# Performance work log

Measured on AMD Instinct MI355X. Metric: run time of the kernel, lower is better.

Reference implementation:

```python
import jax, jax.numpy as jnp
import numpy as np

EMBED = 768
HEADS = 12
DEPTH = 12
FEAT = 2048


def _ln(x, w, b, eps=1e-6):
    m = x.mean(-1, keepdims=True)
    v = ((x - m) ** 2).mean(-1, keepdims=True)
    return (x - m) * jax.lax.rsqrt(v + eps) * w + b


def _var_attn(x, mbias, Wqkv, bqkv, Wp, bp, h, f):
    # x: (B, N, D) with N = 1 + f*n ; mbias: (B, N) additive mask (0 or -100)
    B, N, D = x.shape
    d = D // h
    n = (N - 1) // f
    scale = d ** -0.5
    qkv = x @ Wqkv.T + bqkv
    q, k, v = jnp.split(qkv, 3, axis=-1)
    hd = lambda t: t.reshape(B, N, h, d).transpose(0, 2, 1, 3)  # (B,h,N,d)
    q = hd(q) * scale
    k = hd(k)
    v = hd(v)
    # cls token attends to everything
    cls_sim = jnp.einsum('bhd,bhjd->bhj', q[:, :, 0], k) + mbias[:, None, :]
    cls_out = jnp.einsum('bhj,bhjd->bhd', jax.nn.softmax(cls_sim, axis=-1), v)[:, :, None, :]
    # spatial tokens attend within their frame plus the cls token
    q_ = q[:, :, 1:].reshape(B, h, f, n, d)
    k_ = jnp.concatenate([jnp.broadcast_to(k[:, :, None, 0:1, :], (B, h, f, 1, d)),
                          k[:, :, 1:].reshape(B, h, f, n, d)], axis=3)
    v_ = jnp.concatenate([jnp.broadcast_to(v[:, :, None, 0:1, :], (B, h, f, 1, d)),
                          v[:, :, 1:].reshape(B, h, f, n, d)], axis=3)
    mcat = jnp.concatenate([jnp.broadcast_to(mbias[:, 0][:, None, None], (B, f, 1)),
                            mbias[:, 1:].reshape(B, f, n)], axis=2)  # (B,f,n+1)
    sim = jnp.einsum('bhfid,bhfjd->bhfij', q_, k_) + mcat[:, None, :, None, :]
    out = jnp.einsum('bhfij,bhfjd->bhfid', jax.nn.softmax(sim, axis=-1), v_)
    out = out.reshape(B, h, f * n, d)
    out = jnp.concatenate([cls_out, out], axis=2).transpose(0, 2, 1, 3).reshape(B, N, D)
    return out @ Wp.T + bp


def setup_inputs() -> dict:
    key = jax.random.key(0)
    ks = jax.random.split(key, 12)
    B, F, L = 256, 4, 20
    std = 0.02
    p = {}
    p['x'] = jax.random.normal(ks[0], (B, F, L, 2054), dtype=jnp.float32)
    p['x_mask'] = jax.random.randint(ks[1], (B, F, L), 0, 2, dtype=jnp.int32)
    p['obj_W'] = (jax.random.normal(ks[2], (EMBED, FEAT)) * std).astype(jnp.float32)
    p['obj_b'] = jnp.zeros((EMBED,), jnp.float32)
    p['pos_W'] = (jax.random.normal(ks[3], (EMBED, 6)) * std).astype(jnp.float32)
    p['pos_b'] = jnp.zeros((EMBED,), jnp.float32)
    p['cls_token'] = (jax.random.normal(ks[4], (1, 1, EMBED)) * std).astype(jnp.float32)
    p['cls_pos'] = (jax.random.normal(ks[5], (1, L + 1, EMBED)) * std).astype(jnp.float32)
    p['temporal_embed'] = jnp.zeros((1, F, EMBED), jnp.float32)
    p['ln1_w'] = jnp.ones((DEPTH, EMBED), jnp.float32)
    p['ln1_b'] = jnp.zeros((DEPTH, EMBED), jnp.float32)
    p['ln2_w'] = jnp.ones((DEPTH, EMBED), jnp.float32)
    p['ln2_b'] = jnp.zeros((DEPTH, EMBED), jnp.float32)
    p['qkv_W'] = (jax.random.normal(ks[6], (DEPTH, 3 * EMBED, EMBED)) * std).astype(jnp.float32)
    p['qkv_b'] = jnp.zeros((DEPTH, 3 * EMBED), jnp.float32)
    p['ap_W'] = (jax.random.normal(ks[7], (DEPTH, EMBED, EMBED)) * std).astype(jnp.float32)
    p['ap_b'] = jnp.zeros((DEPTH, EMBED), jnp.float32)
    p['fc1_W'] = (jax.random.normal(ks[8], (DEPTH, 4 * EMBED, EMBED)) * std).astype(jnp.float32)
    p['fc1_b'] = jnp.zeros((DEPTH, 4 * EMBED), jnp.float32)
    p['fc2_W'] = (jax.random.normal(ks[9], (DEPTH, EMBED, 4 * EMBED)) * std).astype(jnp.float32)
    p['fc2_b'] = jnp.zeros((DEPTH, EMBED), jnp.float32)
    p['proj_W'] = (jax.random.normal(ks[10], (256, EMBED)) * std).astype(jnp.float32)
    return p


def reference(x, x_mask, obj_W, obj_b, pos_W, pos_b, cls_token, cls_pos, temporal_embed,
              ln1_w, ln1_b, ln2_w, ln2_b, qkv_W, qkv_b, ap_W, ap_b,
              fc1_W, fc1_b, fc2_W, fc2_b, proj_W):
    B, F, L, _ = x.shape
    tok = x[..., :FEAT] @ obj_W.T + obj_b + (x[..., FEAT:] @ pos_W.T + pos_b)
    tok = tok.reshape(B, F * L, EMBED)
    m = x_mask.reshape(B, F * L).astype(tok.dtype)
    tok = jnp.concatenate([jnp.broadcast_to(cls_token, (B, 1, EMBED)), tok], axis=1)
    m = jnp.concatenate([jnp.ones((B, 1), tok.dtype), m], axis=1)
    mbias = (m - 1.0) * 100.0  # 0 for valid, -100 for padded
    pos_total = jnp.concatenate([cls_pos[:, 0:1, :], jnp.repeat(temporal_embed, L, axis=1)], axis=1)
    tok = tok + pos_total

    def body(xc, p):
        l1w, l1b, qW, qb, aW, ab, l2w, l2b, f1W, f1b, f2W, f2b = p
        a = _var_attn(_ln(xc, l1w, l1b), mbias, qW, qb, aW, ab, HEADS, F)
        xr = xc + a
        xc = xr + (jax.nn.gelu(_ln(xr, l2w, l2b) @ f1W.T + f1b, approximate=False) @ f2W.T + f2b)
        return xc, None

    tok, _ = jax.lax.scan(body, tok, (ln1_w, ln1_b, qkv_W, qkv_b, ap_W, ap_b,
                                      ln2_w, ln2_b, fc1_W, fc1_b, fc2_W, fc2_b))
    return tok @ proj_W.T, mbias
```

## Files before the change

### kernel.cpp

```cpp
#include <hip/hip_runtime.h>

typedef __bf16 bf16;
typedef __bf16 bf16x8 __attribute__((ext_vector_type(8)));
typedef float f32x4 __attribute__((ext_vector_type(4)));

#define EMBED 768
#define HEADS 12
#define DEPTH 12
#define B_ 256
#define F_ 4
#define L_ 20
#define NTOK 81
#define ROWS (B_ * NTOK)
#define SROWS (B_ * F_ * L_)

#define GLOAD16(g, l)                                                              \
    __builtin_amdgcn_global_load_lds((const __attribute__((address_space(1))) void*)(g), \
                                     (__attribute__((address_space(3))) void*)(l), 16, 0, 0)

__device__ __forceinline__ float fast_gelu(float v) {
    float x = v * 0.70710678118654752f;
    float ax = fabsf(x);
    float t = __fdividef(1.f, fmaf(0.3275911f, ax, 1.f));
    float p = ((((1.061405429f * t - 1.453152027f) * t + 1.421413741f) * t -
                0.284496736f) * t + 0.254829592f) * t;
    float e = __expf(-ax * ax);
    float erfv = copysignf(1.f - p * e, x);
    return 0.5f * v * (1.f + erfv);
}

__global__ __launch_bounds__(256) void repack_kernel(const float* __restrict__ x,
                                                     bf16* __restrict__ xr) {
    int row = blockIdx.x;
    const float* src = x + (size_t)row * 2054;
    bf16* dst = xr + (size_t)row * 2048;
    int t = threadIdx.x;
    int e0 = t * 8;
    bf16 tmp[8];
#pragma unroll
    for (int i = 0; i < 4; ++i) {
        float2 v = *(const float2*)&src[e0 + 2 * i];
        tmp[2 * i] = (bf16)v.x;
        tmp[2 * i + 1] = (bf16)v.y;
    }
    *(uint4*)&dst[e0] = *(const uint4*)tmp;
}

__global__ __launch_bounds__(256) void w2bf_kernel(const float* __restrict__ src,
                                                   bf16* __restrict__ dst) {
    size_t i = ((size_t)blockIdx.x * 256 + threadIdx.x) * 8;
    float4 a = *(const float4*)&src[i];
    float4 b = *(const float4*)&src[i + 4];
    bf16 t[8] = {(bf16)a.x, (bf16)a.y, (bf16)a.z, (bf16)a.w,
                 (bf16)b.x, (bf16)b.y, (bf16)b.z, (bf16)b.w};
    *(uint4*)&dst[i] = *(const uint4*)t;
}

template <int FUSE, bool ROWMAP, typename CT>
__global__ __launch_bounds__(256) void gemm_bb(const bf16* __restrict__ A, int lda,
                                               const bf16* __restrict__ W,
                                               const float* __restrict__ bias,
                                               const bf16* __restrict__ R,
                                               CT* __restrict__ C, int N, int K) {
    __shared__ __align__(16) char smem[32768];

    const int tid = threadIdx.x;
    const int lane = tid & 63;
    const int wv = tid >> 6;
    const int wm = (wv & 1) * 64;
    const int wn = (wv >> 1) * 64;
    const int lr = lane & 15;
    const int lq = lane >> 4;

    const int GX = gridDim.x;
    const int nwg = GX * gridDim.y;
    const int flat = blockIdx.y * GX + blockIdx.x;
    const int xcd = flat & 7, pos = flat >> 3;
    const int qc = nwg >> 3, rc = nwg & 7;
    const int wg = (xcd < rc ? xcd * (qc + 1) : rc * (qc + 1) + (xcd - rc) * qc) + pos;
    const int n0 = (wg % GX) * 128;
    const int m0 = (wg / GX) * 128;

    const int srow = lane >> 3;
    const int scol = 8 * ((lane & 7) ^ srow);
    const bf16* aB = A + (size_t)(m0 + srow) * lda + scol;
    const bf16* wB = W + (size_t)(n0 + srow) * K + scol;

    bf16* As = (bf16*)smem;
    bf16* Ws = (bf16*)(smem + 16384);

    f32x4 acc[4][4];
#pragma unroll
    for (int i = 0; i < 4; ++i)
#pragma unroll
        for (int j = 0; j < 4; ++j) acc[i][j] = (f32x4){0.f, 0.f, 0.f, 0.f};

    const int swz = (lr & 7) << 4;

    for (int k0 = 0; k0 < K; k0 += 64) {
#pragma unroll
        for (int i = 0; i < 4; ++i) {
            const int ch = wv * 4 + i;
            GLOAD16(aB + (size_t)(ch * 8) * lda + k0, smem + ch * 1024);
            GLOAD16(wB + (size_t)(ch * 8) * K + k0, smem + 16384 + ch * 1024);
        }
        __syncthreads();
#pragma unroll
        for (int kk = 0; kk < 2; ++kk) {
            const int co = (((kk << 6) | (lq << 4)) ^ swz) >> 1;
            bf16x8 af[4], bw[4];
#pragma unroll
            for (int t = 0; t < 4; ++t) {
                af[t] = *(const bf16x8*)&As[(wm + t * 16 + lr) * 64 + co];
                bw[t] = *(const bf16x8*)&Ws[(wn + t * 16 + lr) * 64 + co];
            }
#pragma unroll
            for (int mi = 0; mi < 4; ++mi)
#pragma unroll
                for (int ni = 0; ni < 4; ++ni)
                    acc[mi][ni] = __builtin_amdgcn_mfma_f32_16x16x32_bf16(af[mi], bw[ni],
                                                                          acc[mi][ni], 0, 0, 0);
        }
        __syncthreads();
    }

    float* patch = (float*)(smem + wv * 4352);
    float bv4[4];
#pragma unroll
    for (int ni = 0; ni < 4; ++ni) bv4[ni] = bias ? bias[n0 + wn + ni * 16 + lr] : 0.f;
    const int rr = lane >> 3;
    const int c8 = (lane & 7) * 8;
#pragma unroll
    for (int mi = 0; mi < 4; ++mi) {
#pragma unroll
        for (int ni = 0; ni < 4; ++ni)
#pragma unroll
            for (int r = 0; r < 4; ++r)
                patch[(lq * 4 + r) * 68 + ni * 16 + lr] = acc[mi][ni][r] + bv4[ni];
#pragma unroll
        for (int hf = 0; hf < 2; ++hf) {
            int row = rr + hf * 8;
            float v[8];
            *(float4*)&v[0] = *(const float4*)&patch[row * 68 + c8];
            *(float4*)&v[4] = *(const float4*)&patch[row * 68 + c8 + 4];
            int grow = m0 + wm + mi * 16 + row;
            int gcol = n0 + wn + c8;
            if (FUSE == 1) {
#pragma unroll
                for (int q = 0; q < 8; ++q) v[q] = fast_gelu(v[q]);
            }
            if (FUSE == 2) {
                bf16x8 rv = *(const bf16x8*)&R[(size_t)grow * N + gcol];
#pragma unroll
                for (int q = 0; q < 8; ++q) v[q] += (float)rv[q];
            }
            int orow = grow;
            if (ROWMAP) orow = grow + grow / 80 + 1;
            if constexpr (sizeof(CT) == 2) {
                bf16 ob[8];
#pragma unroll
                for (int q = 0; q < 8; ++q) ob[q] = (bf16)v[q];
                *(uint4*)&C[(size_t)orow * N + gcol] = *(const uint4*)ob;
            } else {
                *(float4*)&C[(size_t)orow * N + gcol] = *(const float4*)&v[0];
                *(float4*)&C[(size_t)orow * N + gcol + 4] = *(const float4*)&v[4];
            }
        }
    }
}

template <int FUSE, bool ROWMAP, typename CT>
__global__ __launch_bounds__(256) void gemm_bt(const bf16* __restrict__ A, int lda,
                                               const float* __restrict__ W,
                                               const float* __restrict__ bias,
                                               const bf16* __restrict__ R,
                                               CT* __restrict__ C, int N, int K) {
    __shared__ __align__(16) bf16 As[128][32];
    __shared__ __align__(16) bf16 Ws[128][32];

    const int tid = threadIdx.x;
    const int lane = tid & 63;
    const int wv = tid >> 6;
    const int wm = (wv & 1) * 64;
    const int wn = (wv >> 1) * 64;
    const int lr = lane & 15;
    const int lq = lane >> 4;
    const int m0 = blockIdx.x * 128;
    const int n0 = blockIdx.y * 128;

    f32x4 acc[4][4];
#pragma unroll
    for (int i = 0; i < 4; ++i)
#pragma unroll
        for (int j = 0; j < 4; ++j) acc[i][j] = (f32x4){0.f, 0.f, 0.f, 0.f};

    for (int k0 = 0; k0 < K; k0 += 32) {
#pragma unroll
        for (int i = 0; i < 2; ++i) {
            int c = tid + 256 * i;
            int row = c >> 2;
            int kc = (c & 3) * 8;
            *(uint4*)&As[row][kc] = *(const uint4*)&A[(size_t)(m0 + row) * lda + k0 + kc];
        }
#pragma unroll
        for (int i = 0; i < 4; ++i) {
            int c = tid + 256 * i;
            int row = c >> 3;
            int kc = (c & 7) * 4;
            float4 v = *(const float4*)&W[(size_t)(n0 + row) * K + k0 + kc];
            bf16 wb[4] = {(bf16)v.x, (bf16)v.y, (bf16)v.z, (bf16)v.w};
            *(uint2*)&Ws[row][kc] = *(const uint2*)wb;
        }
        __syncthreads();
        bf16x8 af[4], bf_[4];
#pragma unroll
        for (int t = 0; t < 4; ++t) {
            af[t] = *(const bf16x8*)&As[wm + t * 16 + lr][lq * 8];
            bf_[t] = *(const bf16x8*)&Ws[wn + t * 16 + lr][lq * 8];
        }
#pragma unroll
        for (int mi = 0; mi < 4; ++mi)
#pragma unroll
            for (int ni = 0; ni < 4; ++ni)
                acc[mi][ni] = __builtin_amdgcn_mfma_f32_16x16x32_bf16(af[mi], bf_[ni],
                                                                      acc[mi][ni], 0, 0, 0);
        __syncthreads();
    }

#pragma unroll
    for (int mi = 0; mi < 4; ++mi) {
#pragma unroll
        for (int ni = 0; ni < 4; ++ni) {
            int gcol = n0 + wn + ni * 16 + lr;
            float bv = bias ? bias[gcol] : 0.f;
#pragma unroll
            for (int r = 0; r < 4; ++r) {
                int grow = m0 + wm + mi * 16 + lq * 4 + r;
                float v = acc[mi][ni][r] + bv;
                if (FUSE == 1) v = fast_gelu(v);
                if (FUSE == 2) v += (float)R[(size_t)grow * N + gcol];
                int orow = grow;
                if (ROWMAP) orow = grow + grow / 80 + 1;
                C[(size_t)orow * N + gcol] = (CT)v;
            }
        }
    }
}

__global__ __launch_bounds__(256) void embed_finish(const float* __restrict__ x,
                                                    const float* __restrict__ posW,
                                                    const float* __restrict__ posb,
                                                    const float* __restrict__ temb,
                                                    bf16* __restrict__ tok) {
    int r = blockIdx.x;
    int fr = (r % 80) / 20;
    int orow = r + r / 80 + 1;
    __shared__ float pf[6];
    if (threadIdx.x < 6) pf[threadIdx.x] = x[(size_t)r * 2054 + 2048 + threadIdx.x];
    __syncthreads();
    int t = threadIdx.x;
#pragma unroll
    for (int i = 0; i < 3; ++i) {
        int c = t + 256 * i;
        float v = posb[c] + temb[fr * EMBED + c];
#pragma unroll
        for (int j = 0; j < 6; ++j) v += pf[j] * posW[c * 6 + j];
        size_t idx = (size_t)orow * EMBED + c;
        tok[idx] = (bf16)((float)tok[idx] + v);
    }
}

__global__ __launch_bounds__(256) void cls_mbias_kernel(const float* __restrict__ cls_tok,
                                                        const float* __restrict__ cls_pos,
                                                        const int* __restrict__ xmask,
                                                        bf16* __restrict__ tok,
                                                        float* __restrict__ mbias,
                                                        float* __restrict__ out1) {
    int b = blockIdx.x;
    int t = threadIdx.x;
#pragma unroll
    for (int i = 0; i < 3; ++i) {
        int c = t + 256 * i;
        tok[(size_t)(b * NTOK) * EMBED + c] = (bf16)(cls_tok[c] + cls_pos[c]);
    }
    if (t < NTOK) {
        float mv = (t == 0) ? 0.f : ((float)xmask[b * 80 + t - 1] - 1.f) * 100.f;
        mbias[b * NTOK + t] = mv;
        out1[b * NTOK + t] = mv;
    }
}

__global__ __launch_bounds__(256) void ln_kernel(const bf16* __restrict__ X,
                                                 const float* __restrict__ w,
                                                 const float* __restrict__ b,
                                                 bf16* __restrict__ Y) {
    int half = threadIdx.x >> 7;
    int row = blockIdx.x * 2 + half;
    int tt = threadIdx.x & 127;
    float xv[8];
    float s = 0.f, ss = 0.f;
    if (tt < 96) {
        bf16x8 v8 = *(const bf16x8*)&X[(size_t)row * EMBED + tt * 8];
#pragma unroll
        for (int i = 0; i < 8; ++i) {
            float v = (float)v8[i];
            xv[i] = v;
            s += v;
            ss += v * v;
        }
    }
#pragma unroll
    for (int off = 32; off; off >>= 1) {
        s += __shfl_down(s, off);
        ss += __shfl_down(ss, off);
    }
    __shared__ float ws_s[4], ws_q[4];
    int wv = threadIdx.x >> 6, lane = threadIdx.x & 63;
    if (lane == 0) { ws_s[wv] = s; ws_q[wv] = ss; }
    __syncthreads();
    s = ws_s[half * 2] + ws_s[half * 2 + 1];
    ss = ws_q[half * 2] + ws_q[half * 2 + 1];
    float mean = s * (1.f / 768.f);
    float var = ss * (1.f / 768.f) - mean * mean;
    float inv = rsqrtf(fmaxf(var, 0.f) + 1e-6f);
    if (tt < 96) {
        float4 w0 = *(const float4*)&w[tt * 8];
        float4 w1 = *(const float4*)&w[tt * 8 + 4];
        float4 b0 = *(const float4*)&b[tt * 8];
        float4 b1 = *(const float4*)&b[tt * 8 + 4];
        float wr[8] = {w0.x, w0.y, w0.z, w0.w, w1.x, w1.y, w1.z, w1.w};
        float br[8] = {b0.x, b0.y, b0.z, b0.w, b1.x, b1.y, b1.z, b1.w};
        bf16 ob[8];
#pragma unroll
        for (int i = 0; i < 8; ++i) ob[i] = (bf16)((xv[i] - mean) * inv * wr[i] + br[i]);
        *(uint4*)&Y[(size_t)row * EMBED + tt * 8] = *(const uint4*)ob;
    }
}

__global__ __launch_bounds__(256) void attn_kernel(const bf16* __restrict__ qkv,
                                                   const float* __restrict__ mbias,
                                                   bf16* __restrict__ aout) {
    int bh = blockIdx.x;
    int b = bh / HEADS, h = bh % HEADS;
    __shared__ __align__(16) float Qf[NTOK][68];
    __shared__ __align__(16) float Kf[NTOK][68];
    __shared__ __align__(16) bf16 Vs[NTOK][72];
    __shared__ float S[80][22];
    __shared__ float Sc[96];
    __shared__ float MB[NTOK];
    const size_t base = (size_t)(b * NTOK) * 2304 + h * 64;
    int t = threadIdx.x;

    for (int ch = t; ch < NTOK * 8; ch += 256) {
        int r = ch >> 3, c8 = (ch & 7) * 8;
        size_t o = base + (size_t)r * 2304 + c8;
        bf16x8 qv = *(const bf16x8*)&qkv[o];
        bf16x8 kv = *(const bf16x8*)&qkv[o + 768];
        *(uint4*)&Vs[r][c8] = *(const uint4*)&qkv[o + 1536];
        float4 q0 = {(float)qv[0], (float)qv[1], (float)qv[2], (float)qv[3]};
        float4 q1 = {(float)qv[4], (float)qv[5], (float)qv[6], (float)qv[7]};
        float4 k0 = {(float)kv[0], (float)kv[1], (float)kv[2], (float)kv[3]};
        float4 k1 = {(float)kv[4], (float)kv[5], (float)kv[6], (float)kv[7]};
        *(float4*)&Qf[r][c8] = q0;
        *(float4*)&Qf[r][c8 + 4] = q1;
        *(float4*)&Kf[r][c8] = k0;
        *(float4*)&Kf[r][c8 + 4] = k1;
    }
    if (t < NTOK) MB[t] = mbias[b * NTOK + t];
    __syncthreads();

    {
        int qt;
        if (t < 240) {
            qt = 1 + t / 3;
        } else {
            qt = 0;
        }
        float fq[64];
#pragma unroll
        for (int i = 0; i < 16; ++i) {
            float4 v = *(const float4*)&Qf[qt][i * 4];
            fq[4 * i] = v.x; fq[4 * i + 1] = v.y; fq[4 * i + 2] = v.z; fq[4 * i + 3] = v.w;
        }
        if (t < 240) {
            int qi = t / 3, fb = (qi / 20) * 20, kst = t - qi * 3;
            for (int kj = kst; kj < 21; kj += 3) {
                int kt = (kj == 0) ? 0 : fb + kj;
                float acc = 0.f;
#pragma unroll
                for (int i = 0; i < 16; ++i) {
                    float4 kv = *(const float4*)&Kf[kt][i * 4];
                    acc += fq[4 * i] * kv.x + fq[4 * i + 1] * kv.y +
                           fq[4 * i + 2] * kv.z + fq[4 * i + 3] * kv.w;
                }
                S[qi][kj] = acc * 0.125f + MB[kt];
            }
        } else {
            for (int kt = t - 240; kt < NTOK; kt += 16) {
                float acc = 0.f;
#pragma unroll
                for (int i = 0; i < 16; ++i) {
                    float4 kv = *(const float4*)&Kf[kt][i * 4];
                    acc += fq[4 * i] * kv.x + fq[4 * i + 1] * kv.y +
                           fq[4 * i + 2] * kv.z + fq[4 * i + 3] * kv.w;
                }
                Sc[kt] = acc * 0.125f + MB[kt];
            }
        }
    }
    __syncthreads();

    if (t < 80) {
        float mx = -1e30f;
        for (int j = 0; j < 21; ++j) mx = fmaxf(mx, S[t][j]);
        float sum = 0.f;
        for (int j = 0; j < 21; ++j) { float e = __expf(S[t][j] - mx); S[t][j] = e; sum += e; }
        float rs = 1.f / sum;
        for (int j = 0; j < 21; ++j) S[t][j] *= rs;
    } else if (t == 80) {
        float mx = -1e30f;
        for (int j = 0; j < NTOK; ++j) mx = fmaxf(mx, Sc[j]);
        float sum = 0.f;
        for (int j = 0; j < NTOK; ++j) { float e = __expf(Sc[j] - mx); Sc[j] = e; sum += e; }
        float rs = 1.f / sum;
        for (int j = 0; j < NTOK; ++j) Sc[j] *= rs;
    }
    __syncthreads();

    for (int idx = t; idx < NTOK * 8; idx += 256) {
        int r = idx >> 3, c8 = (idx & 7) * 8;
        float acc[8];
#pragma unroll
        for (int q = 0; q < 8; ++q) acc[q] = 0.f;
        if (r == 0) {
            for (int j = 0; j < NTOK; ++j) {
                float w = Sc[j];
                bf16x8 vv = *(const bf16x8*)&Vs[j][c8];
#pragma unroll
                for (int q = 0; q < 8; ++q) acc[q] += w * (float)vv[q];
            }
        } else {
            int qi = r - 1, fb = (qi / 20) * 20;
            {
                float w = S[qi][0];
                bf16x8 vv = *(const bf16x8*)&Vs[0][c8];
#pragma unroll
                for (int q = 0; q < 8; ++q) acc[q] += w * (float)vv[q];
            }
            for (int j = 1; j < 21; ++j) {
                float w = S[qi][j];
                bf16x8 vv = *(const bf16x8*)&Vs[fb + j][c8];
#pragma unroll
                for (int q = 0; q < 8; ++q) acc[q] += w * (float)vv[q];
            }
        }
        bf16 ob[8];
#pragma unroll
        for (int q = 0; q < 8; ++q) ob[q] = (bf16)acc[q];
        *(uint4*)&aout[(size_t)(b * NTOK + r) * EMBED + h * 64 + c8] = *(const uint4*)ob;
    }
}

extern "C" void kernel_launch(void* const* d_in, const int* in_sizes, int n_in,
                              void* d_out, int out_size, void* d_ws, size_t ws_size,
                              hipStream_t stream) {
    const float* x = (const float*)d_in[0];
    const int* xmask = (const int*)d_in[1];
    const float* objW = (const float*)d_in[2];
    const float* objb = (const float*)d_in[3];
    const float* posW = (const float*)d_in[4];
    const float* posb = (const float*)d_in[5];
    const float* clsT = (const float*)d_in[6];
    const float* clsP = (const float*)d_in[7];
    const float* temb = (const float*)d_in[8];
    const float* ln1w = (const float*)d_in[9];
    const float* ln1b = (const float*)d_in[10];
    const float* ln2w = (const float*)d_in[11];
    const float* ln2b = (const float*)d_in[12];
    const float* qkvW = (const float*)d_in[13];
    const float* qkvb = (const float*)d_in[14];
    const float* apW = (const float*)d_in[15];
    const float* apb = (const float*)d_in[16];
    const float* f1W = (const float*)d_in[17];
    const float* f1b = (const float*)d_in[18];
    const float* f2W = (const float*)d_in[19];
    const float* f2b = (const float*)d_in[20];
    const float* projW = (const float*)d_in[21];

    char* ws = (char*)d_ws;
    bf16* tok = (bf16*)(ws);
    bf16* s1 = (bf16*)(ws + (size_t)(32 << 20));
    float* mb = (float*)(ws + (size_t)(64 << 20));
    bf16* big = (bf16*)(ws + (size_t)(65 << 20));
    float* out0 = (float*)d_out;
    float* out1 = out0 + (size_t)ROWS * 256;

    const size_t WOFF = (size_t)192 << 20;
    const size_t E_OBJ = (size_t)768 * 2048;
    const size_t E_QKV = (size_t)DEPTH * 2304 * 768;
    const size_t E_AP = (size_t)DEPTH * 768 * 768;
    const size_t E_FC = (size_t)DEPTH * 3072 * 768;
    const size_t E_PROJ = (size_t)256 * 768;
    const size_t WTOT = (E_OBJ + E_QKV + E_AP + 2 * E_FC + E_PROJ) * 2;
    const bool bigws = ws_size >= WOFF + WTOT;

    if (bigws) {
        bf16* objW16 = (bf16*)(ws + WOFF);
        bf16* qkvW16 = objW16 + E_OBJ;
        bf16* apW16 = qkvW16 + E_QKV;
        bf16* fc1W16 = apW16 + E_AP;
        bf16* fc2W16 = fc1W16 + E_FC;
        bf16* projW16 = fc2W16 + E_FC;

        w2bf_kernel<<<(int)(E_OBJ / 2048), 256, 0, stream>>>(objW, objW16);
        w2bf_kernel<<<(int)(E_QKV / 2048), 256, 0, stream>>>(qkvW, qkvW16);
        w2bf_kernel<<<(int)(E_AP / 2048), 256, 0, stream>>>(apW, apW16);
        w2bf_kernel<<<(int)(E_FC / 2048), 256, 0, stream>>>(f1W, fc1W16);
        w2bf_kernel<<<(int)(E_FC / 2048), 256, 0, stream>>>(f2W, fc2W16);
        w2bf_kernel<<<(int)(E_PROJ / 2048), 256, 0, stream>>>(projW, projW16);

        repack_kernel<<<SROWS, 256, 0, stream>>>(x, big);
        gemm_bb<0, true, bf16><<<dim3(EMBED / 128, SROWS / 128), 256, 0, stream>>>(
            big, 2048, objW16, objb, nullptr, tok, EMBED, 2048);
        embed_finish<<<SROWS, 256, 0, stream>>>(x, posW, posb, temb, tok);
        cls_mbias_kernel<<<B_, 256, 0, stream>>>(clsT, clsP, xmask, tok, mb, out1);

        for (int l = 0; l < DEPTH; ++l) {
            ln_kernel<<<ROWS / 2, 256, 0, stream>>>(tok, ln1w + l * EMBED, ln1b + l * EMBED, s1);
            gemm_bb<0, false, bf16><<<dim3(2304 / 128, ROWS / 128), 256, 0, stream>>>(
                s1, EMBED, qkvW16 + (size_t)l * 2304 * 768, qkvb + l * 2304, nullptr, big,
                2304, EMBED);
            attn_kernel<<<B_ * HEADS, 256, 0, stream>>>(big, mb, s1);
            gemm_bb<2, false, bf16><<<dim3(EMBED / 128, ROWS / 128), 256, 0, stream>>>(
                s1, EMBED, apW16 + (size_t)l * 768 * 768, apb + l * EMBED, tok, tok, EMBED,
                EMBED);
            ln_kernel<<<ROWS / 2, 256, 0, stream>>>(tok, ln2w + l * EMBED, ln2b + l * EMBED, s1);
            gemm_bb<1, false, bf16><<<dim3(3072 / 128, ROWS / 128), 256, 0, stream>>>(
                s1, EMBED, fc1W16 + (size_t)l * 3072 * 768, f1b + l * 3072, nullptr, big,
                3072, EMBED);
            gemm_bb<2, false, bf16><<<dim3(EMBED / 128, ROWS / 128), 256, 0, stream>>>(
                big, 3072, fc2W16 + (size_t)l * 3072 * 768, f2b + l * EMBED, tok, tok, EMBED,
                3072);
        }

        gemm_bb<0, false, float><<<dim3(256 / 128, ROWS / 128), 256, 0, stream>>>(
            tok, EMBED, projW16, nullptr, nullptr, out0, 256, EMBED);
    } else {
        repack_kernel<<<SROWS, 256, 0, stream>>>(x, big);
        gemm_bt<0, true, bf16><<<dim3(SROWS / 128, EMBED / 128), 256, 0, stream>>>(
            big, 2048, objW, objb, nullptr, tok, EMBED, 2048);
        embed_finish<<<SROWS, 256, 0, stream>>>(x, posW, posb, temb, tok);
        cls_mbias_kernel<<<B_, 256, 0, stream>>>(clsT, clsP, xmask, tok, mb, out1);

        for (int l = 0; l < DEPTH; ++l) {
            ln_kernel<<<ROWS / 2, 256, 0, stream>>>(tok, ln1w + l * EMBED, ln1b + l * EMBED, s1);
            gemm_bt<0, false, bf16><<<dim3(ROWS / 128, 2304 / 128), 256, 0, stream>>>(
                s1, EMBED, qkvW + (size_t)l * 2304 * EMBED, qkvb + l * 2304, nullptr, big,
                2304, EMBED);
            attn_kernel<<<B_ * HEADS, 256, 0, stream>>>(big, mb, s1);
            gemm_bt<2, false, bf16><<<dim3(ROWS / 128, EMBED / 128), 256, 0, stream>>>(
                s1, EMBED, apW + (size_t)l * EMBED * EMBED, apb + l * EMBED, tok, tok, EMBED,
                EMBED);
            ln_kernel<<<ROWS / 2, 256, 0, stream>>>(tok, ln2w + l * EMBED, ln2b + l * EMBED, s1);
            gemm_bt<1, false, bf16><<<dim3(ROWS / 128, 3072 / 128), 256, 0, stream>>>(
                s1, EMBED, f1W + (size_t)l * 3072 * EMBED, f1b + l * 3072, nullptr, big, 3072,
                EMBED);
            gemm_bt<2, false, bf16><<<dim3(ROWS / 128, EMBED / 128), 256, 0, stream>>>(
                big, 3072, f2W + (size_t)l * EMBED * 3072, f2b + l * EMBED, tok, tok, EMBED,
                3072);
        }

        gemm_bt<0, false, float><<<dim3(ROWS / 128, 256 / 128), 256, 0, stream>>>(
            tok, EMBED, projW, nullptr, nullptr, out0, 256, EMBED);
    }
}
```

Baseline: 7.406 ms.

## Add 256x256-tile 512-thread GEMM with XCD-aware block remap for transformer layers

Introduces a new bf16 MFMA GEMM kernel, gemm_256. It uses 256x256 output tiles, 8 waves, a double-buffered 128KB LDS staging area filled by direct global-to-LDS loads, and a blockIdx remap that groups consecutive tiles onto the same XCD. All embedding, QKV, attention-projection and MLP GEMMs switch to it. The larger tiles raise arithmetic intensity and operand reuse per block, and the remap aims for better L2 locality. The trade-off is fewer blocks in flight, roughly one per CU given the LDS use, so less latency hiding, plus a larger accumulator register footprint.

```diff
diff --git a/kernel.cpp b/kernel.cpp
--- a/kernel.cpp
+++ b/kernel.cpp
@@ -54,6 +54,154 @@
     bf16 t[8] = {(bf16)a.x, (bf16)a.y, (bf16)a.z, (bf16)a.w,
                  (bf16)b.x, (bf16)b.y, (bf16)b.z, (bf16)b.w};
     *(uint4*)&dst[i] = *(const uint4*)t;
+}
+
+template <int FUSE, bool ROWMAP, typename CT>
+__global__ __launch_bounds__(512, 2) void gemm_256(const bf16* __restrict__ A, int lda,
+                                                   const bf16* __restrict__ W,
+                                                   const float* __restrict__ bias,
+                                                   const bf16* __restrict__ R,
+                                                   CT* __restrict__ C, int N, int K) {
+    __shared__ __align__(16) char smem[131072];
+
+    const int tid = threadIdx.x;
+    const int lane = tid & 63;
+    const int wv = tid >> 6;
+    const int wm = (wv >> 2) * 128;
+    const int wn = (wv & 3) * 64;
+    const int lr = lane & 15;
+    const int lq = lane >> 4;
+
+    const int GX = gridDim.x;
+    const int nwg = GX * gridDim.y;
+    const int flat = blockIdx.y * GX + blockIdx.x;
+    const int xcd = flat & 7, pos = flat >> 3;
+    const int qc = nwg >> 3, rc = nwg & 7;
+    const int wg = (xcd < rc ? xcd * (qc + 1) : rc * (qc + 1) + (xcd - rc) * qc) + pos;
+    const int n0 = (wg % GX) * 256;
+    const int m0 = (wg / GX) * 256;
+
+    const int srow = lane >> 3;
+    const int scol = 8 * ((lane & 7) ^ srow);
+    const bf16* aP[4];
+    const bf16* wP[4];
+#pragma unroll
+    for (int i = 0; i < 4; ++i) {
+        aP[i] = A + (size_t)(m0 + wv * 32 + i * 8 + srow) * lda + scol;
+        wP[i] = W + (size_t)(n0 + wv * 32 + i * 8 + srow) * K + scol;
+    }
+
+    f32x4 acc[8][4];
+#pragma unroll
+    for (int i = 0; i < 8; ++i)
+#pragma unroll
+        for (int j = 0; j < 4; ++j) acc[i][j] = (f32x4){0.f, 0.f, 0.f, 0.f};
+
+    const int swz = (lr & 7) << 4;
+    const int co0 = (((0 << 6) | (lq << 4)) ^ swz) >> 1;
+    const int co1 = (((1 << 6) | (lq << 4)) ^ swz) >> 1;
+
+    const int nk = K >> 6;
+
+#pragma unroll
+    for (int i = 0; i < 4; ++i) {
+        GLOAD16(aP[i], smem + (wv * 4 + i) * 1024);
+        GLOAD16(wP[i], smem + 32768 + (wv * 4 + i) * 1024);
+    }
+    asm volatile("s_waitcnt vmcnt(0)" ::: "memory");
+    __builtin_amdgcn_sched_barrier(0);
+    __builtin_amdgcn_s_barrier();
+
+    int c = 0;
+    for (int t = 0; t < nk; ++t) {
+        if (t + 1 < nk) {
+            const int koff = (t + 1) << 6;
+            char* dst = smem + (c ^ 1) * 65536 + (wv * 4) * 1024;
+#pragma unroll
+            for (int i = 0; i < 4; ++i) {
+                GLOAD16(aP[i] + koff, dst + i * 1024);
+                GLOAD16(wP[i] + koff, dst + 32768 + i * 1024);
+            }
+            __builtin_amdgcn_sched_barrier(0);
+        }
+        {
+            const bf16* As_ = (const bf16*)(smem + c * 65536);
+            const bf16* Bs_ = (const bf16*)(smem + c * 65536 + 32768);
+            bf16x8 bw0[4], bw1[4];
+#pragma unroll
+            for (int ni = 0; ni < 4; ++ni) {
+                const int br = (wn + ni * 16 + lr) * 64;
+                bw0[ni] = *(const bf16x8*)&Bs_[br + co0];
+                bw1[ni] = *(const bf16x8*)&Bs_[br + co1];
+            }
+            __builtin_amdgcn_s_setprio(1);
+#pragma unroll
+            for (int mi = 0; mi < 8; ++mi) {
+                const int ar = (wm + mi * 16 + lr) * 64;
+                bf16x8 a0 = *(const bf16x8*)&As_[ar + co0];
+                bf16x8 a1 = *(const bf16x8*)&As_[ar + co1];
+#pragma unroll
+                for (int ni = 0; ni < 4; ++ni) {
+                    acc[mi][ni] =
+                        __builtin_amdgcn_mfma_f32_16x16x32_bf16(a0, bw0[ni], acc[mi][ni], 0, 0, 0);
+                    acc[mi][ni] =
+                        __builtin_amdgcn_mfma_f32_16x16x32_bf16(a1, bw1[ni], acc[mi][ni], 0, 0, 0);
+                }
+            }
+            __builtin_amdgcn_s_setprio(0);
+        }
+        if (t + 1 < nk) {
+            asm volatile("s_waitcnt vmcnt(0)" ::: "memory");
+            __builtin_amdgcn_sched_barrier(0);
+            __builtin_amdgcn_s_barrier();
+        }
+        c ^= 1;
+    }
+
+    __builtin_amdgcn_s_barrier();
+    float* patch = (float*)(smem + wv * 4352);
+    float bv4[4];
+#pragma unroll
+    for (int ni = 0; ni < 4; ++ni) bv4[ni] = bias ? bias[n0 + wn + ni * 16 + lr] : 0.f;
+    const int rr = lane >> 3;
+    const int c8 = (lane & 7) * 8;
+#pragma unroll
+    for (int mi = 0; mi < 8; ++mi) {
+#pragma unroll
+        for (int ni = 0; ni < 4; ++ni)
+#pragma unroll
+            for (int r = 0; r < 4; ++r)
+                patch[(lq * 4 + r) * 68 + ni * 16 + lr] = acc[mi][ni][r] + bv4[ni];
+#pragma unroll
+        for (int hf = 0; hf < 2; ++hf) {
+            int row = rr + hf * 8;
+            float v[8];
+            *(float4*)&v[0] = *(const float4*)&patch[row * 68 + c8];
+            *(float4*)&v[4] = *(const float4*)&patch[row * 68 + c8 + 4];
+            int grow = m0 + wm + mi * 16 + row;
+            int gcol = n0 + wn + c8;
+            if (FUSE == 1) {
+#pragma unroll
+                for (int q = 0; q < 8; ++q) v[q] = fast_gelu(v[q]);
+            }
+            if (FUSE == 2) {
+                bf16x8 rv = *(const bf16x8*)&R[(size_t)grow * N + gcol];
+#pragma unroll
+                for (int q = 0; q < 8; ++q) v[q] += (float)rv[q];
+            }
+            int orow = grow;
+            if (ROWMAP) orow = grow + grow / 80 + 1;
+            if constexpr (sizeof(CT) == 2) {
+                bf16 ob[8];
+#pragma unroll
+                for (int q = 0; q < 8; ++q) ob[q] = (bf16)v[q];
+                *(uint4*)&C[(size_t)orow * N + gcol] = *(const uint4*)ob;
+            } else {
+                *(float4*)&C[(size_t)orow * N + gcol] = *(const float4*)&v[0];
+                *(float4*)&C[(size_t)orow * N + gcol + 4] = *(const float4*)&v[4];
+            }
+        }
+    }
 }
 
 template <int FUSE, bool ROWMAP, typename CT>
@@ -370,12 +518,7 @@
     __syncthreads();
 
     {
-        int qt;
-        if (t < 240) {
-            qt = 1 + t / 3;
-        } else {
-            qt = 0;
-        }
+        int qt = (t < 240) ? 1 + t / 3 : 0;
         float fq[64];
 #pragma unroll
         for (int i = 0; i < 16; ++i) {
@@ -520,25 +663,25 @@
         w2bf_kernel<<<(int)(E_PROJ / 2048), 256, 0, stream>>>(projW, projW16);
 
         repack_kernel<<<SROWS, 256, 0, stream>>>(x, big);
-        gemm_bb<0, true, bf16><<<dim3(EMBED / 128, SROWS / 128), 256, 0, stream>>>(
+        gemm_256<0, true, bf16><<<dim3(EMBED / 256, SROWS / 256), 512, 0, stream>>>(
             big, 2048, objW16, objb, nullptr, tok, EMBED, 2048);
         embed_finish<<<SROWS, 256, 0, stream>>>(x, posW, posb, temb, tok);
         cls_mbias_kernel<<<B_, 256, 0, stream>>>(clsT, clsP, xmask, tok, mb, out1);
 
         for (int l = 0; l < DEPTH; ++l) {
             ln_kernel<<<ROWS / 2, 256, 0, stream>>>(tok, ln1w + l * EMBED, ln1b + l * EMBED, s1);
-            gemm_bb<0, false, bf16><<<dim3(2304 / 128, ROWS / 128), 256, 0, stream>>>(
+            gemm_256<0, false, bf16><<<dim3(2304 / 256, ROWS / 256), 512, 0, stream>>>(
                 s1, EMBED, qkvW16 + (size_t)l * 2304 * 768, qkvb + l * 2304, nullptr, big,
                 2304, EMBED);
             attn_kernel<<<B_ * HEADS, 256, 0, stream>>>(big, mb, s1);
-            gemm_bb<2, false, bf16><<<dim3(EMBED / 128, ROWS / 128), 256, 0, stream>>>(
+            gemm_256<2, false, bf16><<<dim3(EMBED / 256, ROWS / 256), 512, 0, stream>>>(
                 s1, EMBED, apW16 + (size_t)l * 768 * 768, apb + l * EMBED, tok, tok, EMBED,
                 EMBED);
             ln_kernel<<<ROWS / 2, 256, 0, stream>>>(tok, ln2w + l * EMBED, ln2b + l * EMBED, s1);
-            gemm_bb<1, false, bf16><<<dim3(3072 / 128, ROWS / 128), 256, 0, stream>>>(
+            gemm_256<1, false, bf16><<<dim3(3072 / 256, ROWS / 256), 512, 0, stream>>>(
                 s1, EMBED, fc1W16 + (size_t)l * 3072 * 768, f1b + l * 3072, nullptr, big,
                 3072, EMBED);
-            gemm_bb<2, false, bf16><<<dim3(EMBED / 128, ROWS / 128), 256, 0, stream>>>(
+            gemm_256<2, false, bf16><<<dim3(EMBED / 256, ROWS / 256), 512, 0, stream>>>(
                 big, 3072, fc2W16 + (size_t)l * 3072 * 768, f2b + l * EMBED, tok, tok, EMBED,
                 3072);
         }
```

Result: faster. 6.180 ms (-16.5%).
